# Kernel optimization log

Measured on AMD Instinct MI355X. Metric: run time of the kernel, lower is better.

The kernel has to match this reference:

```python
import jax, jax.numpy as jnp
import numpy as np

N_NODES = 100000
N_EDGES = 1600000
D_IN, D_H, D_OUT = 512, 128, 64
BN_EPS = 1e-5


def setup_inputs() -> dict:
    key = jax.random.key(0)
    ks = jax.random.split(key, 8)
    x = jax.random.normal(ks[0], (N_NODES, D_IN), dtype=jnp.float32)
    # COO sparse normalized adjacency
    row = jnp.sort(jax.random.randint(ks[1], (N_EDGES,), 0, N_NODES))
    col = jax.random.randint(ks[2], (N_EDGES,), 0, N_NODES)
    adj_vals = jax.random.uniform(ks[3], (N_EDGES,), dtype=jnp.float32) / 16.0
    # GraphConvolution params (xavier_uniform weight, zero bias)
    lim0 = float(np.sqrt(6.0 / (D_IN + D_H)))
    lim1 = float(np.sqrt(6.0 / (D_H + D_OUT)))
    W0 = jax.random.uniform(ks[4], (D_IN, D_H), minval=-lim0, maxval=lim0, dtype=jnp.float32)
    W1 = jax.random.uniform(ks[5], (D_H, D_OUT), minval=-lim1, maxval=lim1, dtype=jnp.float32)
    b0 = jnp.zeros((D_H,), dtype=jnp.float32)
    b1 = jnp.zeros((D_OUT,), dtype=jnp.float32)
    return {"x": x, "W0": W0, "b0": b0, "W1": W1, "b1": b1,
            "adj_vals": adj_vals, "row": row, "col": col}


def _spmm(vals, row, col, h, n):
    # (sparse adj) @ h : gather source rows, scale by edge value, scatter-add to dest
    return jax.ops.segment_sum(vals[:, None] * h[col], row, num_segments=n)


def reference(x, W0, b0, W1, b1, adj_vals, row, col):
    n = x.shape[0]
    # layer 0: adj @ (x @ W0) + b0  (dropout is identity in eval mode)
    h = _spmm(adj_vals, row, col, x @ W0, n) + b0
    h = jax.nn.relu(h)
    # BatchNorm1d(affine=False, track_running_stats=False): batch stats, biased var
    mean = jnp.mean(h, axis=0)
    var = jnp.mean(jnp.square(h - mean), axis=0)
    h = (h - mean) * jax.lax.rsqrt(var + BN_EPS)
    # layer 1: adj @ (h @ W1) + b1
    return _spmm(adj_vals, row, col, h @ W1, n) + b1
```

## Files before the change

kernel.cpp:

```cpp
#include <hip/hip_runtime.h>
#include <cstdint>
#include <cstddef>

#define D_IN  512
#define D_H   128
#define D_OUT 64

typedef __attribute__((ext_vector_type(8))) short bf16x8;
typedef __attribute__((ext_vector_type(4))) float f32x4;

__device__ __forceinline__ float bf2f(unsigned short u) {
  union { unsigned int i; float f; } v; v.i = ((unsigned int)u) << 16; return v.f;
}
__device__ __forceinline__ unsigned short f2bf(float f) {
  union { unsigned int i; float f; } v; v.f = f;
  unsigned int r = v.i + 0x7FFFu + ((v.i >> 16) & 1u);
  return (unsigned short)(r >> 16);
}

#define OFF_RP    0u
#define OFF_W0T   400384u
#define OFF_W1TP  531456u
#define OFF_SACC  547840u
#define OFF_MEAN  548864u
#define OFF_ISTD  549376u
#define OFF_CVEC  549888u
#define OFF_H     550912u
#define END_H     26150912u
#define END_HW    38950912u

__global__ void k_zero(float* __restrict__ sacc) { sacc[threadIdx.x] = 0.f; }

__global__ void k_rowptr(const int* __restrict__ row, int* __restrict__ rp,
                         int n, int e) {
  int i = blockIdx.x * blockDim.x + threadIdx.x;
  if (i > n) return;
  int lo = 0, hi = e;
  while (lo < hi) { int mid = (lo + hi) >> 1; if (row[mid] < i) lo = mid + 1; else hi = mid; }
  rp[i] = lo;
}

__global__ void k_transpose_w0(const float* __restrict__ W0,
                               unsigned short* __restrict__ W0t) {
  int idx = blockIdx.x * blockDim.x + threadIdx.x;
  int k = idx & (D_IN - 1);
  int n = idx >> 9;
  W0t[n * D_IN + k] = f2bf(W0[k * D_H + n]);
}

__global__ __launch_bounds__(256) void k_gemm1(const float* __restrict__ A,
                                               const unsigned short* __restrict__ Bt,
                                               unsigned short* __restrict__ C,
                                               int M) {
  __shared__ unsigned short Ash[4 * 128 * 8];
  __shared__ unsigned short Bsh[4 * 128 * 8];
  const int tid  = threadIdx.x;
  const int lane = tid & 63;
  const int wave = tid >> 6;
  const int wm = (wave >> 1) * 64;
  const int wn = (wave & 1) * 64;
  const int m0 = blockIdx.x * 128;
  const int quad = lane >> 4;
  const int l16  = lane & 15;
  f32x4 acc[4][4] = {};

  for (int k0 = 0; k0 < D_IN; k0 += 32) {
    __syncthreads();
#pragma unroll
    for (int i = 0; i < 2; ++i) {
      int c = tid + i * 256;
      int m = c >> 2, k8 = c & 3;
      int gm = m0 + m; if (gm >= M) gm = M - 1;
      const float* src = &A[(size_t)gm * D_IN + k0 + k8 * 8];
      f32x4 f0 = *(const f32x4*)src;
      f32x4 f1 = *(const f32x4*)(src + 4);
      bf16x8 pk;
#pragma unroll
      for (int j = 0; j < 4; ++j) { pk[j] = (short)f2bf(f0[j]); pk[4 + j] = (short)f2bf(f1[j]); }
      *(bf16x8*)&Ash[(k8 * 128 + m) * 8] = pk;
      *(bf16x8*)&Bsh[(k8 * 128 + m) * 8] =
          *(const bf16x8*)&Bt[(size_t)m * D_IN + k0 + k8 * 8];
    }
    __syncthreads();
    bf16x8 af[4], bfv[4];
#pragma unroll
    for (int mf = 0; mf < 4; ++mf)
      af[mf] = *(const bf16x8*)&Ash[(quad * 128 + (wm + mf * 16 + l16)) * 8];
#pragma unroll
    for (int nf = 0; nf < 4; ++nf)
      bfv[nf] = *(const bf16x8*)&Bsh[(quad * 128 + (wn + nf * 16 + l16)) * 8];
#pragma unroll
    for (int mf = 0; mf < 4; ++mf)
#pragma unroll
      for (int nf = 0; nf < 4; ++nf)
        acc[mf][nf] = __builtin_amdgcn_mfma_f32_16x16x32_bf16(af[mf], bfv[nf], acc[mf][nf], 0, 0, 0);
  }
#pragma unroll
  for (int mf = 0; mf < 4; ++mf)
#pragma unroll
    for (int nf = 0; nf < 4; ++nf)
#pragma unroll
      for (int i = 0; i < 4; ++i) {
        int r = m0 + wm + mf * 16 + quad * 4 + i;
        int cc = wn + nf * 16 + l16;
        if (r < M) C[(size_t)r * D_H + cc] = f2bf(acc[mf][nf][i]);
      }
}

__global__ __launch_bounds__(256) void k_spmm1(const unsigned int* __restrict__ xw2,
                                               const float* __restrict__ adj,
                                               const int* __restrict__ col,
                                               const int* __restrict__ rp,
                                               const float* __restrict__ b0,
                                               unsigned int* __restrict__ h2,
                                               int n) {
  int node = blockIdx.x * 4 + (threadIdx.x >> 6);
  if (node >= n) return;
  int l = threadIdx.x & 63;
  int e0 = rp[node], e1 = rp[node + 1];
  float a0 = 0.f, a1 = 0.f;
  int e = e0;
  for (; e + 4 <= e1; e += 4) {
    int c0 = col[e], c1 = col[e + 1], c2 = col[e + 2], c3 = col[e + 3];
    float v0 = adj[e], v1 = adj[e + 1], v2 = adj[e + 2], v3 = adj[e + 3];
    unsigned int p0 = xw2[(size_t)c0 * 64 + l];
    unsigned int p1 = xw2[(size_t)c1 * 64 + l];
    unsigned int p2 = xw2[(size_t)c2 * 64 + l];
    unsigned int p3 = xw2[(size_t)c3 * 64 + l];
    a0 += v0 * bf2f((unsigned short)(p0 & 0xFFFF)); a1 += v0 * bf2f((unsigned short)(p0 >> 16));
    a0 += v1 * bf2f((unsigned short)(p1 & 0xFFFF)); a1 += v1 * bf2f((unsigned short)(p1 >> 16));
    a0 += v2 * bf2f((unsigned short)(p2 & 0xFFFF)); a1 += v2 * bf2f((unsigned short)(p2 >> 16));
    a0 += v3 * bf2f((unsigned short)(p3 & 0xFFFF)); a1 += v3 * bf2f((unsigned short)(p3 >> 16));
  }
  for (; e < e1; ++e) {
    int c = col[e];
    float v = adj[e];
    unsigned int p = xw2[(size_t)c * 64 + l];
    a0 += v * bf2f((unsigned short)(p & 0xFFFF));
    a1 += v * bf2f((unsigned short)(p >> 16));
  }
  float r0 = fmaxf(a0 + b0[2 * l], 0.f);
  float r1 = fmaxf(a1 + b0[2 * l + 1], 0.f);
  h2[(size_t)node * 64 + l] = ((unsigned int)f2bf(r1) << 16) | (unsigned int)f2bf(r0);
}

__global__ __launch_bounds__(256) void k_stats(const unsigned short* __restrict__ h,
                                               float* __restrict__ sacc, int n) {
  __shared__ float ss[256], sq[256];
  int t = threadIdx.x;
  int f = t & 127, half = t >> 7;
  float s = 0.f, q = 0.f;
  for (int r = blockIdx.x * 2 + half; r < n; r += gridDim.x * 2) {
    float v = bf2f(h[(size_t)r * D_H + f]);
    s += v; q += v * v;
  }
  ss[t] = s; sq[t] = q;
  __syncthreads();
  if (t < 128) {
    atomicAdd(&sacc[f],       ss[t] + ss[t + 128]);
    atomicAdd(&sacc[128 + f], sq[t] + sq[t + 128]);
  }
}

__global__ void k_redstats(const float* __restrict__ sacc,
                           float* __restrict__ mean, float* __restrict__ istd, int n) {
  int f = threadIdx.x;
  float m = sacc[f] / (float)n;
  float var = sacc[128 + f] / (float)n - m * m;
  if (var < 0.f) var = 0.f;
  mean[f] = m;
  istd[f] = rsqrtf(var + 1e-5f);
}

__global__ void k_prep(const float* __restrict__ W1,
                       const float* __restrict__ mean, const float* __restrict__ istd,
                       unsigned short* __restrict__ W1tp, float* __restrict__ cvec) {
  int t = threadIdx.x;
  for (int idx = t; idx < D_OUT * D_H; idx += 256) {
    int nn = idx >> 7, k = idx & 127;
    W1tp[nn * D_H + k] = f2bf(istd[k] * W1[k * D_OUT + nn]);
  }
  if (t < D_OUT) {
    float a = 0.f;
    for (int k = 0; k < D_H; ++k) a += mean[k] * istd[k] * W1[k * D_OUT + t];
    cvec[t] = -a;
  }
}

__global__ __launch_bounds__(256) void k_gemm2(const unsigned short* __restrict__ A,
                                               const unsigned short* __restrict__ Bt,
                                               const float* __restrict__ cvec,
                                               unsigned short* __restrict__ Cout,
                                               int M) {
  __shared__ unsigned short Ash[4 * 128 * 8];
  __shared__ unsigned short Bsh[4 * 64 * 8];
  const int tid  = threadIdx.x;
  const int lane = tid & 63;
  const int wave = tid >> 6;
  const int wm = wave * 32;
  const int m0 = blockIdx.x * 128;
  const int quad = lane >> 4;
  const int l16  = lane & 15;
  f32x4 acc[2][4] = {};

  for (int k0 = 0; k0 < D_H; k0 += 32) {
    __syncthreads();
#pragma unroll
    for (int i = 0; i < 2; ++i) {
      int c = tid + i * 256;
      int m = c >> 2, k8 = c & 3;
      int gm = m0 + m; if (gm >= M) gm = M - 1;
      *(bf16x8*)&Ash[(k8 * 128 + m) * 8] =
          *(const bf16x8*)&A[(size_t)gm * D_H + k0 + k8 * 8];
    }
    {
      int nn = tid >> 2, k8 = tid & 3;
      *(bf16x8*)&Bsh[(k8 * 64 + nn) * 8] =
          *(const bf16x8*)&Bt[(size_t)nn * D_H + k0 + k8 * 8];
    }
    __syncthreads();
    bf16x8 af[2], bfv[4];
#pragma unroll
    for (int mf = 0; mf < 2; ++mf)
      af[mf] = *(const bf16x8*)&Ash[(quad * 128 + (wm + mf * 16 + l16)) * 8];
#pragma unroll
    for (int nf = 0; nf < 4; ++nf)
      bfv[nf] = *(const bf16x8*)&Bsh[(quad * 64 + (nf * 16 + l16)) * 8];
#pragma unroll
    for (int mf = 0; mf < 2; ++mf)
#pragma unroll
      for (int nf = 0; nf < 4; ++nf)
        acc[mf][nf] = __builtin_amdgcn_mfma_f32_16x16x32_bf16(af[mf], bfv[nf], acc[mf][nf], 0, 0, 0);
  }
#pragma unroll
  for (int mf = 0; mf < 2; ++mf)
#pragma unroll
    for (int nf = 0; nf < 4; ++nf)
#pragma unroll
      for (int i = 0; i < 4; ++i) {
        int r = m0 + wm + mf * 16 + quad * 4 + i;
        int cc = nf * 16 + l16;
        if (r < M) Cout[(size_t)r * 64 + cc] = f2bf(acc[mf][nf][i] + cvec[cc]);
      }
}

__global__ __launch_bounds__(256) void k_spmm2(const unsigned int* __restrict__ hw2,
                                               const float* __restrict__ adj,
                                               const int* __restrict__ col,
                                               const int* __restrict__ rp,
                                               const float* __restrict__ b1,
                                               float2* __restrict__ o2,
                                               int n) {
  int node = blockIdx.x * 8 + (threadIdx.x >> 5);
  if (node >= n) return;
  int l = threadIdx.x & 31;
  int e0 = rp[node], e1 = rp[node + 1];
  float a0 = 0.f, a1 = 0.f;
  int e = e0;
  for (; e + 4 <= e1; e += 4) {
    int c0 = col[e], c1 = col[e + 1], c2 = col[e + 2], c3 = col[e + 3];
    float v0 = adj[e], v1 = adj[e + 1], v2 = adj[e + 2], v3 = adj[e + 3];
    unsigned int p0 = hw2[(size_t)c0 * 32 + l];
    unsigned int p1 = hw2[(size_t)c1 * 32 + l];
    unsigned int p2 = hw2[(size_t)c2 * 32 + l];
    unsigned int p3 = hw2[(size_t)c3 * 32 + l];
    a0 += v0 * bf2f((unsigned short)(p0 & 0xFFFF)); a1 += v0 * bf2f((unsigned short)(p0 >> 16));
    a0 += v1 * bf2f((unsigned short)(p1 & 0xFFFF)); a1 += v1 * bf2f((unsigned short)(p1 >> 16));
    a0 += v2 * bf2f((unsigned short)(p2 & 0xFFFF)); a1 += v2 * bf2f((unsigned short)(p2 >> 16));
    a0 += v3 * bf2f((unsigned short)(p3 & 0xFFFF)); a1 += v3 * bf2f((unsigned short)(p3 >> 16));
  }
  for (; e < e1; ++e) {
    int c = col[e];
    float v = adj[e];
    unsigned int p = hw2[(size_t)c * 32 + l];
    a0 += v * bf2f((unsigned short)(p & 0xFFFF));
    a1 += v * bf2f((unsigned short)(p >> 16));
  }
  float2 r; r.x = a0 + b1[2 * l]; r.y = a1 + b1[2 * l + 1];
  o2[(size_t)node * 32 + l] = r;
}

extern "C" void kernel_launch(void* const* d_in, const int* in_sizes, int n_in,
                              void* d_out, int out_size, void* d_ws, size_t ws_size,
                              hipStream_t stream) {
  const float* x   = (const float*)d_in[0];
  const float* W0  = (const float*)d_in[1];
  const float* b0  = (const float*)d_in[2];
  const float* W1  = (const float*)d_in[3];
  const float* b1  = (const float*)d_in[4];
  const float* adj = (const float*)d_in[5];
  const int* row = (const int*)d_in[6];
  const int* col = (const int*)d_in[7];
  const int N = in_sizes[0] / D_IN;
  const int E = in_sizes[5];

  char* ws = (char*)d_ws;
  int*            rp   = (int*)(ws + OFF_RP);
  unsigned short* W0t  = (unsigned short*)(ws + OFF_W0T);
  unsigned short* W1tp = (unsigned short*)(ws + OFF_W1TP);
  float*          sacc = (float*)(ws + OFF_SACC);
  float*          mean = (float*)(ws + OFF_MEAN);
  float*          istd = (float*)(ws + OFF_ISTD);
  float*          cvec = (float*)(ws + OFF_CVEC);
  unsigned short* h    = (unsigned short*)(ws + OFF_H);

  unsigned short* xw = (unsigned short*)d_out;
  const bool hw_in_ws = (ws_size >= (size_t)END_HW);
  unsigned short* hw   = hw_in_ws ? (unsigned short*)(ws + END_H) : (unsigned short*)d_out;
  float*          outd = hw_in_ws ? (float*)d_out                 : (float*)(ws + OFF_H);

  k_zero<<<1, 256, 0, stream>>>(sacc);
  k_rowptr<<<(N + 1 + 255) / 256, 256, 0, stream>>>(row, rp, N, E);
  k_transpose_w0<<<(D_IN * D_H) / 256, 256, 0, stream>>>(W0, W0t);

  k_gemm1<<<(N + 127) / 128, 256, 0, stream>>>(x, W0t, xw, N);
  k_spmm1<<<(N + 3) / 4, 256, 0, stream>>>((const unsigned int*)xw, adj, col, rp, b0,
                                           (unsigned int*)h, N);

  k_stats<<<512, 256, 0, stream>>>(h, sacc, N);
  k_redstats<<<1, 128, 0, stream>>>(sacc, mean, istd, N);
  k_prep<<<1, 256, 0, stream>>>(W1, mean, istd, W1tp, cvec);

  k_gemm2<<<(N + 127) / 128, 256, 0, stream>>>(h, W1tp, cvec, hw, N);
  k_spmm2<<<(N + 7) / 8, 256, 0, stream>>>((const unsigned int*)hw, adj, col, rp, b1,
                                           (float2*)outd, N);

  if (!hw_in_ws) {
    hipMemcpyAsync(d_out, outd, (size_t)N * D_OUT * sizeof(float),
                   hipMemcpyDeviceToDevice, stream);
  }
}
```

Before: 515.8 us.

## Merge setup kernels, double-buffer gemm1, widen SpMM gather batches, vectorize stats

Three setup kernels (rowptr, W0 transpose, zeroing) become one launch, and the BN-stat reduction is folded into the W1 prep kernel, which cuts launch count. gemm1 now double-buffers LDS and prefetches the next K tile into registers, dropping one barrier per iteration so loads overlap MFMA work. Both SpMM kernels gather 8 edges per batch with masked tails to keep more loads in flight. The stats kernel reads packed bf16 pairs, which uses more registers and shared memory.

```diff
diff --git a/kernel.cpp b/kernel.cpp
--- a/kernel.cpp
+++ b/kernel.cpp
@@ -22,38 +22,37 @@
 #define OFF_W0T   400384u
 #define OFF_W1TP  531456u
 #define OFF_SACC  547840u
-#define OFF_MEAN  548864u
-#define OFF_ISTD  549376u
 #define OFF_CVEC  549888u
 #define OFF_H     550912u
 #define END_H     26150912u
 #define END_HW    38950912u
 
-__global__ void k_zero(float* __restrict__ sacc) { sacc[threadIdx.x] = 0.f; }
-
-__global__ void k_rowptr(const int* __restrict__ row, int* __restrict__ rp,
-                         int n, int e) {
-  int i = blockIdx.x * blockDim.x + threadIdx.x;
-  if (i > n) return;
-  int lo = 0, hi = e;
-  while (lo < hi) { int mid = (lo + hi) >> 1; if (row[mid] < i) lo = mid + 1; else hi = mid; }
-  rp[i] = lo;
-}
-
-__global__ void k_transpose_w0(const float* __restrict__ W0,
-                               unsigned short* __restrict__ W0t) {
-  int idx = blockIdx.x * blockDim.x + threadIdx.x;
-  int k = idx & (D_IN - 1);
-  int n = idx >> 9;
-  W0t[n * D_IN + k] = f2bf(W0[k * D_H + n]);
+__global__ void k_init(const int* __restrict__ row, int* __restrict__ rp,
+                       const float* __restrict__ W0, unsigned short* __restrict__ W0t,
+                       float* __restrict__ sacc, int n, int e, int RB, int TB) {
+  int b = blockIdx.x, t = threadIdx.x;
+  if (b < RB) {
+    int i = b * 256 + t;
+    if (i > n) return;
+    int lo = 0, hi = e;
+    while (lo < hi) { int mid = (lo + hi) >> 1; if (row[mid] < i) lo = mid + 1; else hi = mid; }
+    rp[i] = lo;
+  } else if (b < RB + TB) {
+    int idx = (b - RB) * 256 + t;
+    int k = idx & (D_IN - 1);
+    int nn = idx >> 9;
+    W0t[nn * D_IN + k] = f2bf(W0[k * D_H + nn]);
+  } else {
+    sacc[t] = 0.f;
+  }
 }
 
 __global__ __launch_bounds__(256) void k_gemm1(const float* __restrict__ A,
                                                const unsigned short* __restrict__ Bt,
                                                unsigned short* __restrict__ C,
                                                int M) {
-  __shared__ unsigned short Ash[4 * 128 * 8];
-  __shared__ unsigned short Bsh[4 * 128 * 8];
+  __shared__ unsigned short Ash[2][4 * 128 * 8];
+  __shared__ unsigned short Bsh[2][4 * 128 * 8];
   const int tid  = threadIdx.x;
   const int lane = tid & 63;
   const int wave = tid >> 6;
@@ -64,31 +63,60 @@
   const int l16  = lane & 15;
   f32x4 acc[4][4] = {};
 
-  for (int k0 = 0; k0 < D_IN; k0 += 32) {
+  int am[2], ak[2];
+  const float* aptr[2];
+  const unsigned short* bptr[2];
+#pragma unroll
+  for (int i = 0; i < 2; ++i) {
+    int c = tid + i * 256;
+    am[i] = c >> 2; ak[i] = c & 3;
+    int gm = m0 + am[i]; if (gm >= M) gm = M - 1;
+    aptr[i] = A  + (size_t)gm * D_IN + ak[i] * 8;
+    bptr[i] = Bt + (size_t)am[i] * D_IN + ak[i] * 8;
+  }
+
+  f32x4 areg[2][2];
+  bf16x8 breg[2];
+#pragma unroll
+  for (int i = 0; i < 2; ++i) {
+    areg[i][0] = *(const f32x4*)(aptr[i]);
+    areg[i][1] = *(const f32x4*)(aptr[i] + 4);
+    breg[i]    = *(const bf16x8*)(bptr[i]);
+  }
+
+  const int NIT = D_IN / 32;
+  for (int it = 0; it < NIT; ++it) {
+    const int buf = it & 1;
+    unsigned short* ash = Ash[buf];
+    unsigned short* bsh = Bsh[buf];
+#pragma unroll
+    for (int i = 0; i < 2; ++i) {
+      bf16x8 pk;
+#pragma unroll
+      for (int j = 0; j < 4; ++j) {
+        pk[j]     = (short)f2bf(areg[i][0][j]);
+        pk[4 + j] = (short)f2bf(areg[i][1][j]);
+      }
+      *(bf16x8*)&ash[(ak[i] * 128 + am[i]) * 8] = pk;
+      *(bf16x8*)&bsh[(ak[i] * 128 + am[i]) * 8] = breg[i];
+    }
     __syncthreads();
-#pragma unroll
-    for (int i = 0; i < 2; ++i) {
-      int c = tid + i * 256;
-      int m = c >> 2, k8 = c & 3;
-      int gm = m0 + m; if (gm >= M) gm = M - 1;
-      const float* src = &A[(size_t)gm * D_IN + k0 + k8 * 8];
-      f32x4 f0 = *(const f32x4*)src;
-      f32x4 f1 = *(const f32x4*)(src + 4);
-      bf16x8 pk;
-#pragma unroll
-      for (int j = 0; j < 4; ++j) { pk[j] = (short)f2bf(f0[j]); pk[4 + j] = (short)f2bf(f1[j]); }
-      *(bf16x8*)&Ash[(k8 * 128 + m) * 8] = pk;
-      *(bf16x8*)&Bsh[(k8 * 128 + m) * 8] =
-          *(const bf16x8*)&Bt[(size_t)m * D_IN + k0 + k8 * 8];
-    }
-    __syncthreads();
+    if (it + 1 < NIT) {
+      int k0 = (it + 1) * 32;
+#pragma unroll
+      for (int i = 0; i < 2; ++i) {
+        areg[i][0] = *(const f32x4*)(aptr[i] + k0);
+        areg[i][1] = *(const f32x4*)(aptr[i] + k0 + 4);
+        breg[i]    = *(const bf16x8*)(bptr[i] + k0);
+      }
+    }
     bf16x8 af[4], bfv[4];
 #pragma unroll
     for (int mf = 0; mf < 4; ++mf)
-      af[mf] = *(const bf16x8*)&Ash[(quad * 128 + (wm + mf * 16 + l16)) * 8];
+      af[mf] = *(const bf16x8*)&ash[(quad * 128 + (wm + mf * 16 + l16)) * 8];
 #pragma unroll
     for (int nf = 0; nf < 4; ++nf)
-      bfv[nf] = *(const bf16x8*)&Bsh[(quad * 128 + (wn + nf * 16 + l16)) * 8];
+      bfv[nf] = *(const bf16x8*)&bsh[(quad * 128 + (wn + nf * 16 + l16)) * 8];
 #pragma unroll
     for (int mf = 0; mf < 4; ++mf)
 #pragma unroll
@@ -119,70 +147,73 @@
   int l = threadIdx.x & 63;
   int e0 = rp[node], e1 = rp[node + 1];
   float a0 = 0.f, a1 = 0.f;
-  int e = e0;
-  for (; e + 4 <= e1; e += 4) {
-    int c0 = col[e], c1 = col[e + 1], c2 = col[e + 2], c3 = col[e + 3];
-    float v0 = adj[e], v1 = adj[e + 1], v2 = adj[e + 2], v3 = adj[e + 3];
-    unsigned int p0 = xw2[(size_t)c0 * 64 + l];
-    unsigned int p1 = xw2[(size_t)c1 * 64 + l];
-    unsigned int p2 = xw2[(size_t)c2 * 64 + l];
-    unsigned int p3 = xw2[(size_t)c3 * 64 + l];
-    a0 += v0 * bf2f((unsigned short)(p0 & 0xFFFF)); a1 += v0 * bf2f((unsigned short)(p0 >> 16));
-    a0 += v1 * bf2f((unsigned short)(p1 & 0xFFFF)); a1 += v1 * bf2f((unsigned short)(p1 >> 16));
-    a0 += v2 * bf2f((unsigned short)(p2 & 0xFFFF)); a1 += v2 * bf2f((unsigned short)(p2 >> 16));
-    a0 += v3 * bf2f((unsigned short)(p3 & 0xFFFF)); a1 += v3 * bf2f((unsigned short)(p3 >> 16));
-  }
-  for (; e < e1; ++e) {
-    int c = col[e];
-    float v = adj[e];
-    unsigned int p = xw2[(size_t)c * 64 + l];
-    a0 += v * bf2f((unsigned short)(p & 0xFFFF));
-    a1 += v * bf2f((unsigned short)(p >> 16));
+  for (int e = e0; e < e1; e += 8) {
+    int   idx[8]; float w[8];
+#pragma unroll
+    for (int j = 0; j < 8; ++j) {
+      int ee = e + j;
+      int ec = ee < e1 ? ee : e0;
+      idx[j] = col[ec];
+      w[j] = ee < e1 ? adj[ec] : 0.f;
+    }
+#pragma unroll
+    for (int j = 0; j < 8; ++j) {
+      unsigned int p = xw2[(size_t)idx[j] * 64 + l];
+      a0 += w[j] * bf2f((unsigned short)(p & 0xFFFF));
+      a1 += w[j] * bf2f((unsigned short)(p >> 16));
+    }
   }
   float r0 = fmaxf(a0 + b0[2 * l], 0.f);
   float r1 = fmaxf(a1 + b0[2 * l + 1], 0.f);
   h2[(size_t)node * 64 + l] = ((unsigned int)f2bf(r1) << 16) | (unsigned int)f2bf(r0);
 }
 
-__global__ __launch_bounds__(256) void k_stats(const unsigned short* __restrict__ h,
+__global__ __launch_bounds__(256) void k_stats(const unsigned int* __restrict__ h2,
                                                float* __restrict__ sacc, int n) {
-  __shared__ float ss[256], sq[256];
+  __shared__ float sA[256], sB[256], qA[256], qB[256];
   int t = threadIdx.x;
-  int f = t & 127, half = t >> 7;
-  float s = 0.f, q = 0.f;
-  for (int r = blockIdx.x * 2 + half; r < n; r += gridDim.x * 2) {
-    float v = bf2f(h[(size_t)r * D_H + f]);
-    s += v; q += v * v;
-  }
-  ss[t] = s; sq[t] = q;
+  int f2 = t & 63, rg = t >> 6;
+  float s0 = 0.f, s1 = 0.f, q0 = 0.f, q1 = 0.f;
+  for (int r = blockIdx.x * 4 + rg; r < n; r += gridDim.x * 4) {
+    unsigned int p = h2[(size_t)r * 64 + f2];
+    float v0 = bf2f((unsigned short)(p & 0xFFFF));
+    float v1 = bf2f((unsigned short)(p >> 16));
+    s0 += v0; s1 += v1; q0 += v0 * v0; q1 += v1 * v1;
+  }
+  sA[t] = s0; sB[t] = s1; qA[t] = q0; qB[t] = q1;
   __syncthreads();
+  if (t < 64) {
+    float S0 = sA[t] + sA[t + 64] + sA[t + 128] + sA[t + 192];
+    float S1 = sB[t] + sB[t + 64] + sB[t + 128] + sB[t + 192];
+    float Q0 = qA[t] + qA[t + 64] + qA[t + 128] + qA[t + 192];
+    float Q1 = qB[t] + qB[t + 64] + qB[t + 128] + qB[t + 192];
+    atomicAdd(&sacc[2 * t],           S0);
+    atomicAdd(&sacc[2 * t + 1],       S1);
+    atomicAdd(&sacc[128 + 2 * t],     Q0);
+    atomicAdd(&sacc[128 + 2 * t + 1], Q1);
+  }
+}
+
+__global__ void k_prep2(const float* __restrict__ sacc, const float* __restrict__ W1,
+                        unsigned short* __restrict__ W1tp, float* __restrict__ cvec,
+                        int n) {
+  __shared__ float mean_s[128], istd_s[128];
+  int t = threadIdx.x;
   if (t < 128) {
-    atomicAdd(&sacc[f],       ss[t] + ss[t + 128]);
-    atomicAdd(&sacc[128 + f], sq[t] + sq[t + 128]);
-  }
-}
-
-__global__ void k_redstats(const float* __restrict__ sacc,
-                           float* __restrict__ mean, float* __restrict__ istd, int n) {
-  int f = threadIdx.x;
-  float m = sacc[f] / (float)n;
-  float var = sacc[128 + f] / (float)n - m * m;
-  if (var < 0.f) var = 0.f;
-  mean[f] = m;
-  istd[f] = rsqrtf(var + 1e-5f);
-}
-
-__global__ void k_prep(const float* __restrict__ W1,
-                       const float* __restrict__ mean, const float* __restrict__ istd,
-                       unsigned short* __restrict__ W1tp, float* __restrict__ cvec) {
-  int t = threadIdx.x;
+    float m = sacc[t] / (float)n;
+    float var = sacc[128 + t] / (float)n - m * m;
+    if (var < 0.f) var = 0.f;
+    mean_s[t] = m;
+    istd_s[t] = rsqrtf(var + 1e-5f);
+  }
+  __syncthreads();
   for (int idx = t; idx < D_OUT * D_H; idx += 256) {
     int nn = idx >> 7, k = idx & 127;
-    W1tp[nn * D_H + k] = f2bf(istd[k] * W1[k * D_OUT + nn]);
+    W1tp[nn * D_H + k] = f2bf(istd_s[k] * W1[k * D_OUT + nn]);
   }
   if (t < D_OUT) {
     float a = 0.f;
-    for (int k = 0; k < D_H; ++k) a += mean[k] * istd[k] * W1[k * D_OUT + t];
+    for (int k = 0; k < D_H; ++k) a += mean_s[k] * istd_s[k] * W1[k * D_OUT + t];
     cvec[t] = -a;
   }
 }
@@ -256,25 +287,21 @@
   int l = threadIdx.x & 31;
   int e0 = rp[node], e1 = rp[node + 1];
   float a0 = 0.f, a1 = 0.f;
-  int e = e0;
-  for (; e + 4 <= e1; e += 4) {
-    int c0 = col[e], c1 = col[e + 1], c2 = col[e + 2], c3 = col[e + 3];
-    float v0 = adj[e], v1 = adj[e + 1], v2 = adj[e + 2], v3 = adj[e + 3];
-    unsigned int p0 = hw2[(size_t)c0 * 32 + l];
-    unsigned int p1 = hw2[(size_t)c1 * 32 + l];
-    unsigned int p2 = hw2[(size_t)c2 * 32 + l];
-    unsigned int p3 = hw2[(size_t)c3 * 32 + l];
-    a0 += v0 * bf2f((unsigned short)(p0 & 0xFFFF)); a1 += v0 * bf2f((unsigned short)(p0 >> 16));
-    a0 += v1 * bf2f((unsigned short)(p1 & 0xFFFF)); a1 += v1 * bf2f((unsigned short)(p1 >> 16));
-    a0 += v2 * bf2f((unsigned short)(p2 & 0xFFFF)); a1 += v2 * bf2f((unsigned short)(p2 >> 16));
-    a0 += v3 * bf2f((unsigned short)(p3 & 0xFFFF)); a1 += v3 * bf2f((unsigned short)(p3 >> 16));
-  }
-  for (; e < e1; ++e) {
-    int c = col[e];
-    float v = adj[e];
-    unsigned int p = hw2[(size_t)c * 32 + l];
-    a0 += v * bf2f((unsigned short)(p & 0xFFFF));
-    a1 += v * bf2f((unsigned short)(p >> 16));
+  for (int e = e0; e < e1; e += 8) {
+    int   idx[8]; float w[8];
+#pragma unroll
+    for (int j = 0; j < 8; ++j) {
+      int ee = e + j;
+      int ec = ee < e1 ? ee : e0;
+      idx[j] = col[ec];
+      w[j] = ee < e1 ? adj[ec] : 0.f;
+    }
+#pragma unroll
+    for (int j = 0; j < 8; ++j) {
+      unsigned int p = hw2[(size_t)idx[j] * 32 + l];
+      a0 += w[j] * bf2f((unsigned short)(p & 0xFFFF));
+      a1 += w[j] * bf2f((unsigned short)(p >> 16));
+    }
   }
   float2 r; r.x = a0 + b1[2 * l]; r.y = a1 + b1[2 * l + 1];
   o2[(size_t)node * 32 + l] = r;
@@ -299,8 +326,6 @@
   unsigned short* W0t  = (unsigned short*)(ws + OFF_W0T);
   unsigned short* W1tp = (unsigned short*)(ws + OFF_W1TP);
   float*          sacc = (float*)(ws + OFF_SACC);
-  float*          mean = (float*)(ws + OFF_MEAN);
-  float*          istd = (float*)(ws + OFF_ISTD);
   float*          cvec = (float*)(ws + OFF_CVEC);
   unsigned short* h    = (unsigned short*)(ws + OFF_H);
 
@@ -309,18 +334,15 @@
   unsigned short* hw   = hw_in_ws ? (unsigned short*)(ws + END_H) : (unsigned short*)d_out;
   float*          outd = hw_in_ws ? (float*)d_out                 : (float*)(ws + OFF_H);
 
-  k_zero<<<1, 256, 0, stream>>>(sacc);
-  k_rowptr<<<(N + 1 + 255) / 256, 256, 0, stream>>>(row, rp, N, E);
-  k_transpose_w0<<<(D_IN * D_H) / 256, 256, 0, stream>>>(W0, W0t);
+  const int RB = (N + 1 + 255) / 256;
+  const int TB = (D_IN * D_H) / 256;
+  k_init<<<RB + TB + 1, 256, 0, stream>>>(row, rp, W0, W0t, sacc, N, E, RB, TB);
 
   k_gemm1<<<(N + 127) / 128, 256, 0, stream>>>(x, W0t, xw, N);
   k_spmm1<<<(N + 3) / 4, 256, 0, stream>>>((const unsigned int*)xw, adj, col, rp, b0,
                                            (unsigned int*)h, N);
-
-  k_stats<<<512, 256, 0, stream>>>(h, sacc, N);
-  k_redstats<<<1, 128, 0, stream>>>(sacc, mean, istd, N);
-  k_prep<<<1, 256, 0, stream>>>(W1, mean, istd, W1tp, cvec);
-
+  k_stats<<<512, 256, 0, stream>>>((const unsigned int*)h, sacc, N);
+  k_prep2<<<1, 256, 0, stream>>>(sacc, W1, W1tp, cvec, N);
   k_gemm2<<<(N + 127) / 128, 256, 0, stream>>>(h, W1tp, cvec, hw, N);
   k_spmm2<<<(N + 7) / 8, 256, 0, stream>>>((const unsigned int*)hw, adj, col, rp, b1,
                                            (float2*)outd, N);
```

Result: faster. 489.5 us (-5.1%).
